# Kernel tuning notes

Hardware: AMD Instinct MI355X
Metric: run time of the kernel (lower is better)

Reference implementation:

```python
import jax, jax.numpy as jnp
import numpy as np

# Standard SMPL kinematic tree (24 joints); parents[0] = -1 (root)
PARENTS = np.array([-1, 0, 0, 0, 1, 2, 3, 4, 5, 6, 7, 8, 9, 9, 9, 12, 13, 14, 16, 17, 18, 19, 20, 21], dtype=np.int32)
B, V, J, NSHAPE, NPOSEBASIS = 512, 6890, 24, 10, 207


def setup_inputs() -> dict:
    key = jax.random.key(0)
    ks = jax.random.split(key, 9)
    poses = jax.random.normal(ks[0], (B, J * 3), dtype=jnp.float32) * 0.2
    shapes = jax.random.normal(ks[1], (B, NSHAPE), dtype=jnp.float32)
    Rh = jax.random.normal(ks[2], (B, 3), dtype=jnp.float32) * 0.2
    Th = jax.random.normal(ks[3], (B, 3), dtype=jnp.float32)
    v_template = jax.random.normal(ks[4], (V, 3), dtype=jnp.float32)
    shapedirs = jax.random.normal(ks[5], (V, 3, NSHAPE), dtype=jnp.float32) * 0.01
    posedirs = jax.random.normal(ks[6], (NPOSEBASIS, V * 3), dtype=jnp.float32) * 0.01
    jr = jax.random.uniform(ks[7], (J, V), dtype=jnp.float32)
    J_regressor = jr / jnp.sum(jr, axis=1, keepdims=True)
    w = jax.random.uniform(ks[8], (V, J), dtype=jnp.float32)
    weights = w / jnp.sum(w, axis=1, keepdims=True)
    return {"poses": poses, "shapes": shapes, "Rh": Rh, "Th": Th,
            "v_template": v_template, "shapedirs": shapedirs, "posedirs": posedirs,
            "J_regressor": J_regressor, "weights": weights}


def batch_rodrigues(rot_vecs):
    # rot_vecs: (N,3) -> (N,3,3); matches smplx batch_rodrigues
    angle = jnp.linalg.norm(rot_vecs + 1e-8, axis=1, keepdims=True)  # (N,1)
    rd = rot_vecs / angle
    cos = jnp.cos(angle)[:, :, None]
    sin = jnp.sin(angle)[:, :, None]
    rx, ry, rz = rd[:, 0], rd[:, 1], rd[:, 2]
    zeros = jnp.zeros_like(rx)
    K = jnp.stack([zeros, -rz, ry, rz, zeros, -rx, -ry, rx, zeros], axis=1).reshape(-1, 3, 3)
    ident = jnp.eye(3, dtype=rot_vecs.dtype)[None]
    return ident + sin * K + (1.0 - cos) * jnp.matmul(K, K)


def smpl_forward(poses, shapes, Rh, Th, v_template, shapedirs, posedirs, J_regressor, weights):
    bn = poses.shape[0]
    # shape blendshapes: v_shaped (B,V,3)
    v_shaped = v_template[None] + jnp.einsum('bl,vdl->bvd', shapes, shapedirs)
    # rest-pose joints (B,J,3)
    Jrest = jnp.einsum('jv,bvd->bjd', J_regressor, v_shaped)
    # per-joint rotation matrices
    rot_mats = batch_rodrigues(poses.reshape(-1, 3)).reshape(bn, J, 3, 3)
    # pose blendshapes
    ident = jnp.eye(3, dtype=poses.dtype)
    pose_feature = (rot_mats[:, 1:] - ident).reshape(bn, -1)  # (B,207)
    v_posed = v_shaped + jnp.matmul(pose_feature, posedirs).reshape(bn, V, 3)
    # kinematic chain rigid transforms
    rel_joints = jnp.concatenate([Jrest[:, :1], Jrest[:, 1:] - Jrest[:, PARENTS[1:]]], axis=1)
    bottom = jnp.tile(jnp.array([0., 0., 0., 1.], dtype=poses.dtype), (bn, J, 1, 1))
    tmats = jnp.concatenate([jnp.concatenate([rot_mats, rel_joints[..., None]], axis=-1), bottom], axis=-2)  # (B,J,4,4)
    chain = [tmats[:, 0]]
    for i in range(1, J):
        chain.append(jnp.matmul(chain[PARENTS[i]], tmats[:, i]))
    transforms = jnp.stack(chain, axis=1)  # (B,J,4,4)
    # remove rest-pose joint location from transforms
    tj = jnp.einsum('bjik,bjk->bji', transforms[:, :, :3, :3], Jrest)
    A = transforms.at[:, :, :3, 3].add(-tj)
    # linear blend skinning
    T = jnp.einsum('vj,bjik->bvik', weights, A)  # (B,V,4,4)
    verts = jnp.einsum('bvik,bvk->bvi', T[:, :, :3, :3], v_posed) + T[:, :, :3, 3]
    # global rotation + translation
    rot = batch_rodrigues(Rh)  # (B,3,3)
    vertices = jnp.einsum('bij,bvj->bvi', rot, verts) + Th[:, None]
    return vertices


def reference(poses, shapes, Rh, Th, v_template, shapedirs, posedirs, J_regressor, weights):
    return smpl_forward(poses, shapes, Rh, Th, v_template, shapedirs, posedirs, J_regressor, weights)
```

## Files before the change

### kernel.cpp

```cpp
#include <hip/hip_runtime.h>


#define BN 512
#define NV 6890
#define NVP 6912
#define NJ 24
#define NS 10
#define NP 207
#define PSTR 208
#define KP 224
#define NPAD 20736
#define BB 8
#define TV 256

#define WS_JSP 0
#define WS_G   6400
#define WS_PF  153856
#define WS_A1  12800
#define WS_A2  127488
#define WS_WT  324096
#define WS_BT  545280
#define FULL_NEED ((size_t)10380288)

typedef unsigned short u16;
typedef short bf16x8 __attribute__((ext_vector_type(8)));
typedef float f32x4  __attribute__((ext_vector_type(4)));

__constant__ int c_par[NJ] = {-1,0,0,0,1,2,3,4,5,6,7,8,9,9,9,12,13,14,16,17,18,19,20,21};

__device__ __forceinline__ u16 f2bf(float f){
    union { float f; unsigned i; } x; x.f = f;
    unsigned r = x.i + 0x7fffu + ((x.i >> 16) & 1u);
    return (u16)(r >> 16);
}

__global__ __launch_bounds__(256) void k_prep(const float* __restrict__ jreg,
                                              const float* __restrict__ vt,
                                              const float* __restrict__ sd,
                                              const float* __restrict__ pd,
                                              const float* __restrict__ wts,
                                              float* __restrict__ ws,
                                              u16* __restrict__ bt,
                                              u16* __restrict__ wt,
                                              int full){
    __shared__ __align__(16) float s_red[4][33];
    __shared__ __align__(16) u16 s_tile[32][65];
    int bid = blockIdx.x;
    int t = threadIdx.x;

    if(bid < 192){
        int j = bid >> 3, s = bid & 7;
        int v0 = s*864, v1 = min(NV, v0+864);
        float acc[33];
        #pragma unroll
        for(int k=0;k<33;k++) acc[k]=0.f;
        for(int v=v0+t; v<v1; v+=256){
            float jr = jreg[j*NV+v];
            #pragma unroll
            for(int d=0;d<3;d++) acc[d] = fmaf(jr, vt[v*3+d], acc[d]);
            const float2* sp = (const float2*)(sd + (size_t)v*30);
            #pragma unroll
            for(int k=0;k<15;k++){
                float2 s2 = sp[k];
                acc[3+2*k]   = fmaf(jr, s2.x, acc[3+2*k]);
                acc[3+2*k+1] = fmaf(jr, s2.y, acc[3+2*k+1]);
            }
        }
        int lane = t & 63, wv = t >> 6;
        #pragma unroll
        for(int k=0;k<33;k++){
            float val = acc[k];
            #pragma unroll
            for(int off=32; off; off>>=1) val += __shfl_down(val, off, 64);
            if(lane==0) s_red[wv][k]=val;
        }
        __syncthreads();
        if(t<33) ws[WS_JSP + (j*8+s)*33 + t] = s_red[0][t]+s_red[1][t]+s_red[2][t]+s_red[3][t];
    } else if(bid < 2460){
        if(!full) return;
        int bid2 = bid - 192;
        int n0 = (bid2 % 324) * 64;
        int k0 = (bid2 / 324) * 32;
        int nl = t & 63, kb = (t>>6)*8;
        int n = n0 + nl;
        #pragma unroll
        for(int i=0;i<8;i++){
            int k = k0 + kb + i;
            float v = 0.f;
            if(n < NV*3){
                if(k < NP)           v = pd[(size_t)k*(NV*3) + n];
                else if(k < NP+NS)   v = sd[(size_t)(n/3)*30 + (n%3)*10 + (k-NP)];
            }
            s_tile[kb+i][nl] = f2bf(v);
        }
        __syncthreads();
        int nl2 = t >> 2, kc = t & 3;
        union { u16 s[8]; uint4 q; } u;
        #pragma unroll
        for(int i=0;i<8;i++) u.s[i] = s_tile[kc*8+i][nl2];
        int ng = n0 + nl2;
        int v = ng/3, d = ng%3;
        int chunk = (k0>>3) + kc;
        *(uint4*)(bt + (((size_t)d*28 + chunk)*NVP + v)*8) = u.q;
    } else {
        if(!full) return;
        int v = (bid - 2460)*256 + t;
        if(v >= NVP) return;
        union { u16 s[32]; uint4 q[4]; } u;
        #pragma unroll
        for(int j=0;j<24;j++) u.s[j] = (v<NV) ? f2bf(wts[(size_t)v*24+j]) : (u16)0;
        #pragma unroll
        for(int j=24;j<32;j++) u.s[j]=0;
        #pragma unroll
        for(int c=0;c<4;c++)
            *(uint4*)(wt + ((size_t)c*NVP + v)*8) = u.q[c];
    }
}

__global__ __launch_bounds__(64) void k_chain(const float* __restrict__ poses,
                                              const float* __restrict__ shapes,
                                              const float* __restrict__ Rh,
                                              float* __restrict__ ws,
                                              u16* __restrict__ a1,
                                              u16* __restrict__ a2,
                                              int full){
    int b = blockIdx.x;
    int t = threadIdx.x;
    __shared__ float R[25][9];
    __shared__ float sh[NS];
    __shared__ float js[792];
    __shared__ float jrest[NJ][3];
    __shared__ float rel[NJ][3];
    __shared__ float chR[NJ][9];
    __shared__ float chT[NJ][3];
    __shared__ float Gs[NJ][12];

    if(t<25){
        float x,y,z;
        if(t<24){ x=poses[b*72+t*3]; y=poses[b*72+t*3+1]; z=poses[b*72+t*3+2]; }
        else    { x=Rh[b*3];         y=Rh[b*3+1];         z=Rh[b*3+2]; }
        float ax=x+1e-8f, ay=y+1e-8f, az=z+1e-8f;
        float ang = sqrtf(ax*ax+ay*ay+az*az);
        float inv = 1.f/ang;
        float rx=x*inv, ry=y*inv, rz=z*inv;
        float s = sinf(ang), c = cosf(ang), oc = 1.f - c;
        R[t][0]=1.f+oc*(-rz*rz-ry*ry); R[t][1]=-s*rz+oc*(rx*ry);      R[t][2]= s*ry+oc*(rx*rz);
        R[t][3]= s*rz+oc*(rx*ry);      R[t][4]=1.f+oc*(-rz*rz-rx*rx); R[t][5]=-s*rx+oc*(ry*rz);
        R[t][6]=-s*ry+oc*(rx*rz);      R[t][7]= s*rx+oc*(ry*rz);      R[t][8]=1.f+oc*(-ry*ry-rx*rx);
    }
    if(t<NS) sh[t]=shapes[b*NS+t];
    for(int idx=t; idx<792; idx+=64){
        int j = idx/33, e = idx%33;
        float a = 0.f;
        #pragma unroll
        for(int s=0;s<8;s++) a += ws[WS_JSP + (j*8+s)*33 + e];
        js[idx]=a;
    }
    __syncthreads();

    for(int idx=t; idx<KP; idx+=64){
        float v = 0.f;
        if(idx<NP){
            int j = 1 + idx/9, e = idx%9;
            v = R[j][e] - ((e==0||e==4||e==8)?1.f:0.f);
        } else if(idx<NP+NS) v = sh[idx-NP];
        if(full){ a1[(((size_t)(idx>>3))*BN + b)*8 + (idx&7)] = f2bf(v); }
        else if(idx<PSTR) ws[WS_PF + b*PSTR + idx] = (idx<NP)?v:0.f;
    }
    if(t<NJ){
        #pragma unroll
        for(int d=0;d<3;d++){
            float a = js[t*33 + d];
            #pragma unroll
            for(int l=0;l<NS;l++) a = fmaf(sh[l], js[t*33 + 3 + d*10 + l], a);
            jrest[t][d]=a;
        }
    }
    __syncthreads();
    if(t<NJ){
        int p = c_par[t];
        #pragma unroll
        for(int d=0;d<3;d++) rel[t][d] = (t==0) ? jrest[0][d] : jrest[t][d]-jrest[p][d];
    }
    __syncthreads();
    if(t<9) chR[0][t]=R[0][t];
    if(t<3) chT[0][t]=rel[0][t];
    __syncthreads();
    for(int i=1;i<NJ;i++){
        if(t<12){
            int r=t>>2, cc=t&3, p=c_par[i];
            if(cc<3){
                chR[i][r*3+cc] = chR[p][r*3+0]*R[i][0*3+cc] + chR[p][r*3+1]*R[i][1*3+cc] + chR[p][r*3+2]*R[i][2*3+cc];
            } else {
                chT[i][r] = chR[p][r*3+0]*rel[i][0] + chR[p][r*3+1]*rel[i][1] + chR[p][r*3+2]*rel[i][2] + chT[p][r];
            }
        }
        __syncthreads();
    }
    if(t<NJ){
        float rg[9];
        #pragma unroll
        for(int k=0;k<9;k++) rg[k]=R[24][k];
        float at[3];
        #pragma unroll
        for(int r=0;r<3;r++){
            float tj = chR[t][r*3+0]*jrest[t][0] + chR[t][r*3+1]*jrest[t][1] + chR[t][r*3+2]*jrest[t][2];
            at[r] = chT[t][r] - tj;
        }
        #pragma unroll
        for(int r=0;r<3;r++){
            #pragma unroll
            for(int cc=0;cc<3;cc++)
                Gs[t][r*4+cc] = rg[r*3+0]*chR[t][0*3+cc] + rg[r*3+1]*chR[t][1*3+cc] + rg[r*3+2]*chR[t][2*3+cc];
            Gs[t][r*4+3] = rg[r*3+0]*at[0] + rg[r*3+1]*at[1] + rg[r*3+2]*at[2];
        }
    }
    __syncthreads();
    if(full){
        for(int idx=t; idx<12*32; idx+=64){
            int e = idx>>5, k = idx&31;
            float v = (k<NJ) ? Gs[k][e] : 0.f;
            a2[((((size_t)e*4)+(k>>3))*BN + b)*8 + (k&7)] = f2bf(v);
        }
    } else if(t<NJ){
        float* g = &ws[WS_G + b*288 + t*12];
        #pragma unroll
        for(int e=0;e<12;e++) g[e] = Gs[t][e];
    }
}

__global__ __launch_bounds__(256) void k_fused(const u16* __restrict__ A1,
                                               const u16* __restrict__ A2,
                                               const u16* __restrict__ WT,
                                               const u16* __restrict__ BT,
                                               const float* __restrict__ vt,
                                               const float* __restrict__ th,
                                               float* __restrict__ out){
    int t = threadIdx.x;
    int w = t>>6, lane = t&63;
    int quad = lane>>4, l16 = lane&15;
    int v = blockIdx.y*64 + w*16 + l16;

    bf16x8 Bf[3][7];
    #pragma unroll
    for(int d=0;d<3;d++)
        #pragma unroll
        for(int s=0;s<7;s++)
            Bf[d][s] = *(const bf16x8*)(BT + (((size_t)d*28 + s*4 + quad)*NVP + v)*8);
    bf16x8 wf = *(const bf16x8*)(WT + ((size_t)quad*NVP + v)*8);
    float vt0=0.f, vt1=0.f, vt2=0.f;
    if(v<NV){ vt0=vt[v*3]; vt1=vt[v*3+1]; vt2=vt[v*3+2]; }
    f32x4 zz = {0.f,0.f,0.f,0.f};

    #pragma unroll 1
    for(int mi=0;mi<8;mi++){
        int m0 = blockIdx.x*128 + mi*16;
        int mrow = m0 + l16;
        f32x4 accP0=zz, accP1=zz, accP2=zz;
        #pragma unroll
        for(int s=0;s<7;s++){
            bf16x8 af = *(const bf16x8*)(A1 + (((size_t)s*4 + quad)*BN + mrow)*8);
            accP0 = __builtin_amdgcn_mfma_f32_16x16x32_bf16(af, Bf[0][s], accP0, 0,0,0);
            accP1 = __builtin_amdgcn_mfma_f32_16x16x32_bf16(af, Bf[1][s], accP1, 0,0,0);
            accP2 = __builtin_amdgcn_mfma_f32_16x16x32_bf16(af, Bf[2][s], accP2, 0,0,0);
        }
        f32x4 accT[12];
        #pragma unroll
        for(int e=0;e<12;e++){
            bf16x8 gf = *(const bf16x8*)(A2 + (((size_t)e*4 + quad)*BN + mrow)*8);
            accT[e] = __builtin_amdgcn_mfma_f32_16x16x32_bf16(gf, wf, zz, 0,0,0);
        }
        if(v < NV){
            #pragma unroll
            for(int r=0;r<4;r++){
                int b = m0 + quad*4 + r;
                float t0 = th[b*3+0], t1 = th[b*3+1], t2 = th[b*3+2];
                float p0 = accP0[r] + vt0;
                float p1 = accP1[r] + vt1;
                float p2 = accP2[r] + vt2;
                float o0 = fmaf(accT[0][r],p0, fmaf(accT[1][r],p1, fmaf(accT[2][r], p2, accT[3][r]))) + t0;
                float o1 = fmaf(accT[4][r],p0, fmaf(accT[5][r],p1, fmaf(accT[6][r], p2, accT[7][r]))) + t1;
                float o2 = fmaf(accT[8][r],p0, fmaf(accT[9][r],p1, fmaf(accT[10][r],p2, accT[11][r]))) + t2;
                float* op = out + ((size_t)b*NV + v)*3;
                op[0]=o0; op[1]=o1; op[2]=o2;
            }
        }
    }
}

__global__ __launch_bounds__(256) void k_main(const float* __restrict__ vt,
                                              const float* __restrict__ sd,
                                              const float* __restrict__ pd,
                                              const float* __restrict__ wts,
                                              const float* __restrict__ th,
                                              const float* __restrict__ shapes,
                                              const float* __restrict__ ws,
                                              float* __restrict__ out){
    __shared__ __align__(16) float pf_s[BB*PSTR];
    __shared__ __align__(16) float g_s[BB*288];
    __shared__ float th_s[BB*3];
    __shared__ float sh_s[BB*NS];
    int tid = threadIdx.x;
    int b0  = blockIdx.y * BB;
    int v   = blockIdx.x * TV + tid;

    for(int i=tid; i<BB*PSTR; i+=TV) pf_s[i] = ws[WS_PF + b0*PSTR + i];
    for(int i=tid; i<BB*288;  i+=TV) g_s[i]  = ws[WS_G  + b0*288  + i];
    if(tid<BB*3)  th_s[tid] = th[b0*3+tid];
    if(tid<BB*NS) sh_s[tid] = shapes[b0*NS+tid];
    __syncthreads();
    if(v>=NV) return;

    float sdv[30];
    {
        const float2* sp = (const float2*)(sd + (size_t)v*30);
        #pragma unroll
        for(int i=0;i<15;i++){ float2 s2 = sp[i]; sdv[2*i]=s2.x; sdv[2*i+1]=s2.y; }
    }
    float vt0=vt[v*3], vt1=vt[v*3+1], vt2=vt[v*3+2];
    float vp[BB][3];
    #pragma unroll
    for(int b=0;b<BB;b++){
        #pragma unroll
        for(int d=0;d<3;d++){
            float a = (d==0)?vt0:((d==1)?vt1:vt2);
            #pragma unroll
            for(int l=0;l<NS;l++) a = fmaf(sh_s[b*NS+l], sdv[d*10+l], a);
            vp[b][d]=a;
        }
    }
    const float* pcol = pd + (size_t)v*3;
    int p=0;
    for(; p<=NP-4; p+=4){
        float pdv[4][3];
        #pragma unroll
        for(int q=0;q<4;q++){
            size_t base = (size_t)(p+q)*(NV*3);
            pdv[q][0]=pcol[base]; pdv[q][1]=pcol[base+1]; pdv[q][2]=pcol[base+2];
        }
        #pragma unroll
        for(int b=0;b<BB;b++){
            float4 f = *(const float4*)&pf_s[b*PSTR+p];
            #pragma unroll
            for(int d=0;d<3;d++)
                vp[b][d] = fmaf(f.x,pdv[0][d], fmaf(f.y,pdv[1][d], fmaf(f.z,pdv[2][d], fmaf(f.w,pdv[3][d], vp[b][d]))));
        }
    }
    for(; p<NP; p++){
        size_t base=(size_t)p*(NV*3);
        float p0=pcol[base], p1=pcol[base+1], p2=pcol[base+2];
        #pragma unroll
        for(int b=0;b<BB;b++){
            float f = pf_s[b*PSTR+p];
            vp[b][0]=fmaf(f,p0,vp[b][0]); vp[b][1]=fmaf(f,p1,vp[b][1]); vp[b][2]=fmaf(f,p2,vp[b][2]);
        }
    }
    float w[24];
    {
        const float4* wp = (const float4*)(wts + (size_t)v*24);
        #pragma unroll
        for(int i=0;i<6;i++){
            float4 u = wp[i];
            w[i*4+0]=u.x; w[i*4+1]=u.y; w[i*4+2]=u.z; w[i*4+3]=u.w;
        }
    }
    #pragma unroll 1
    for(int b=0;b<BB;b++){
        float4 T0=make_float4(0.f,0.f,0.f,0.f), T1=T0, T2=T0;
        #pragma unroll
        for(int j=0;j<NJ;j++){
            float wj = w[j];
            const float4* g = (const float4*)&g_s[b*288 + j*12];
            float4 g0=g[0], g1=g[1], g2=g[2];
            T0.x=fmaf(wj,g0.x,T0.x); T0.y=fmaf(wj,g0.y,T0.y); T0.z=fmaf(wj,g0.z,T0.z); T0.w=fmaf(wj,g0.w,T0.w);
            T1.x=fmaf(wj,g1.x,T1.x); T1.y=fmaf(wj,g1.y,T1.y); T1.z=fmaf(wj,g1.z,T1.z); T1.w=fmaf(wj,g1.w,T1.w);
            T2.x=fmaf(wj,g2.x,T2.x); T2.y=fmaf(wj,g2.y,T2.y); T2.z=fmaf(wj,g2.z,T2.z); T2.w=fmaf(wj,g2.w,T2.w);
        }
        float x=vp[b][0], y=vp[b][1], z=vp[b][2];
        float ox = fmaf(T0.x,x, fmaf(T0.y,y, fmaf(T0.z,z, T0.w))) + th_s[b*3+0];
        float oy = fmaf(T1.x,x, fmaf(T1.y,y, fmaf(T1.z,z, T1.w))) + th_s[b*3+1];
        float oz = fmaf(T2.x,x, fmaf(T2.y,y, fmaf(T2.z,z, T2.w))) + th_s[b*3+2];
        size_t o = ((size_t)(b0+b)*NV + v)*3;
        out[o]=ox; out[o+1]=oy; out[o+2]=oz;
    }
}

extern "C" void kernel_launch(void* const* d_in, const int* in_sizes, int n_in,
                              void* d_out, int out_size, void* d_ws, size_t ws_size,
                              hipStream_t stream){
    const float* poses  = (const float*)d_in[0];
    const float* shapes = (const float*)d_in[1];
    const float* Rh     = (const float*)d_in[2];
    const float* Th     = (const float*)d_in[3];
    const float* vt     = (const float*)d_in[4];
    const float* sd     = (const float*)d_in[5];
    const float* pdirs  = (const float*)d_in[6];
    const float* jreg   = (const float*)d_in[7];
    const float* wts    = (const float*)d_in[8];
    float* ws  = (float*)d_ws;
    float* out = (float*)d_out;
    u16* u = (u16*)d_ws;
    int full = (ws_size >= FULL_NEED) ? 1 : 0;

    hipLaunchKernelGGL(k_prep, dim3(2487), dim3(256), 0, stream,
                       jreg, vt, sd, pdirs, wts, ws, u + WS_BT, u + WS_WT, full);
    hipLaunchKernelGGL(k_chain, dim3(BN), dim3(64), 0, stream, poses, shapes, Rh, ws,
                       u + WS_A1, u + WS_A2, full);
    if(full){
        hipLaunchKernelGGL(k_fused, dim3(BN/128, NVP/64), dim3(256), 0, stream,
                           u + WS_A1, u + WS_A2, u + WS_WT, u + WS_BT, vt, Th, out);
    } else {
        hipLaunchKernelGGL(k_main, dim3((NV+TV-1)/TV, BN/BB), dim3(256), 0, stream,
                           vt, sd, pdirs, wts, Th, shapes, ws, out);
    }
}
```

Before: 137.4 us.

## Parallelize kinematic chain by tree level and pack four batches per block

The chain kernel now computes all joints at the same tree depth together, so it runs 8 level steps instead of 23 serial joint steps with a barrier after each. It also processes four batch items per 256-thread block (one wavefront each), which amortizes the joint-regressor partial-sum reduction over four items. Separately, the prep kernel stages shapedirs rows through shared memory with coalesced float4 loads instead of strided per-thread float2 reads. The staging adds extra block barriers and a large shared buffer that may lower occupancy of the prep kernel.

```diff
diff --git a/kernel.cpp b/kernel.cpp
--- a/kernel.cpp
+++ b/kernel.cpp
@@ -27,6 +27,8 @@
 typedef float f32x4  __attribute__((ext_vector_type(4)));
 
 __constant__ int c_par[NJ] = {-1,0,0,0,1,2,3,4,5,6,7,8,9,9,9,12,13,14,16,17,18,19,20,21};
+__constant__ int c_lvl_joint[23] = {1,2,3, 4,5,6, 7,8,9, 10,11,12,13,14, 15,16,17, 18,19, 20,21, 22,23};
+__constant__ int c_lvl_off[9]    = {0,3,6,9,14,17,19,21,23};
 
 __device__ __forceinline__ u16 f2bf(float f){
     union { float f; unsigned i; } x; x.f = f;
@@ -45,6 +47,7 @@
                                               int full){
     __shared__ __align__(16) float s_red[4][33];
     __shared__ __align__(16) u16 s_tile[32][65];
+    __shared__ __align__(16) float s_sd[256*30];
     int bid = blockIdx.x;
     int t = threadIdx.x;
 
@@ -54,17 +57,22 @@
         float acc[33];
         #pragma unroll
         for(int k=0;k<33;k++) acc[k]=0.f;
-        for(int v=v0+t; v<v1; v+=256){
-            float jr = jreg[j*NV+v];
-            #pragma unroll
-            for(int d=0;d<3;d++) acc[d] = fmaf(jr, vt[v*3+d], acc[d]);
-            const float2* sp = (const float2*)(sd + (size_t)v*30);
-            #pragma unroll
-            for(int k=0;k<15;k++){
-                float2 s2 = sp[k];
-                acc[3+2*k]   = fmaf(jr, s2.x, acc[3+2*k]);
-                acc[3+2*k+1] = fmaf(jr, s2.y, acc[3+2*k+1]);
+        for(int c0=v0; c0<v1; c0+=256){
+            int nv = min(256, v1-c0);
+            int nf4 = (nv*30) >> 2;
+            const float4* src = (const float4*)(sd + (size_t)c0*30);
+            for(int i=t; i<nf4; i+=256) ((float4*)s_sd)[i] = src[i];
+            __syncthreads();
+            if(t<nv){
+                int v = c0 + t;
+                float jr = jreg[j*NV+v];
+                #pragma unroll
+                for(int d=0;d<3;d++) acc[d] = fmaf(jr, vt[v*3+d], acc[d]);
+                const float* sp = &s_sd[t*30];
+                #pragma unroll
+                for(int k=0;k<30;k++) acc[3+k] = fmaf(jr, sp[k], acc[3+k]);
             }
+            __syncthreads();
         }
         int lane = t & 63, wv = t >> 6;
         #pragma unroll
@@ -117,115 +125,131 @@
     }
 }
 
-__global__ __launch_bounds__(64) void k_chain(const float* __restrict__ poses,
-                                              const float* __restrict__ shapes,
-                                              const float* __restrict__ Rh,
-                                              float* __restrict__ ws,
-                                              u16* __restrict__ a1,
-                                              u16* __restrict__ a2,
-                                              int full){
-    int b = blockIdx.x;
-    int t = threadIdx.x;
-    __shared__ float R[25][9];
-    __shared__ float sh[NS];
+__global__ __launch_bounds__(256) void k_chain(const float* __restrict__ poses,
+                                               const float* __restrict__ shapes,
+                                               const float* __restrict__ Rh,
+                                               float* __restrict__ ws,
+                                               u16* __restrict__ a1,
+                                               u16* __restrict__ a2,
+                                               int full){
+    int tid  = threadIdx.x;
+    int w    = tid >> 6;
+    int lane = tid & 63;
+    int b    = blockIdx.x*4 + w;
+
     __shared__ float js[792];
-    __shared__ float jrest[NJ][3];
-    __shared__ float rel[NJ][3];
-    __shared__ float chR[NJ][9];
-    __shared__ float chT[NJ][3];
-    __shared__ float Gs[NJ][12];
-
-    if(t<25){
+    __shared__ float R[4][25][9];
+    __shared__ float sh[4][NS];
+    __shared__ float jrest[4][NJ][3];
+    __shared__ float rel[4][NJ][3];
+    __shared__ float chR[4][NJ][9];
+    __shared__ float chT[4][NJ][3];
+    __shared__ float Gs[4][NJ][12];
+
+    for(int idx=tid; idx<792; idx+=256){
+        int j = idx/33, e = idx%33;
+        float a = 0.f;
+        #pragma unroll
+        for(int s=0;s<8;s++) a += ws[WS_JSP + (j*8+s)*33 + e];
+        js[idx]=a;
+    }
+    if(lane<25){
         float x,y,z;
-        if(t<24){ x=poses[b*72+t*3]; y=poses[b*72+t*3+1]; z=poses[b*72+t*3+2]; }
-        else    { x=Rh[b*3];         y=Rh[b*3+1];         z=Rh[b*3+2]; }
+        if(lane<24){ x=poses[b*72+lane*3]; y=poses[b*72+lane*3+1]; z=poses[b*72+lane*3+2]; }
+        else       { x=Rh[b*3];            y=Rh[b*3+1];            z=Rh[b*3+2]; }
         float ax=x+1e-8f, ay=y+1e-8f, az=z+1e-8f;
         float ang = sqrtf(ax*ax+ay*ay+az*az);
         float inv = 1.f/ang;
         float rx=x*inv, ry=y*inv, rz=z*inv;
         float s = sinf(ang), c = cosf(ang), oc = 1.f - c;
-        R[t][0]=1.f+oc*(-rz*rz-ry*ry); R[t][1]=-s*rz+oc*(rx*ry);      R[t][2]= s*ry+oc*(rx*rz);
-        R[t][3]= s*rz+oc*(rx*ry);      R[t][4]=1.f+oc*(-rz*rz-rx*rx); R[t][5]=-s*rx+oc*(ry*rz);
-        R[t][6]=-s*ry+oc*(rx*rz);      R[t][7]= s*rx+oc*(ry*rz);      R[t][8]=1.f+oc*(-ry*ry-rx*rx);
-    }
-    if(t<NS) sh[t]=shapes[b*NS+t];
-    for(int idx=t; idx<792; idx+=64){
-        int j = idx/33, e = idx%33;
-        float a = 0.f;
-        #pragma unroll
-        for(int s=0;s<8;s++) a += ws[WS_JSP + (j*8+s)*33 + e];
-        js[idx]=a;
-    }
-    __syncthreads();
-
-    for(int idx=t; idx<KP; idx+=64){
+        R[w][lane][0]=1.f+oc*(-rz*rz-ry*ry); R[w][lane][1]=-s*rz+oc*(rx*ry);      R[w][lane][2]= s*ry+oc*(rx*rz);
+        R[w][lane][3]= s*rz+oc*(rx*ry);      R[w][lane][4]=1.f+oc*(-rz*rz-rx*rx); R[w][lane][5]=-s*rx+oc*(ry*rz);
+        R[w][lane][6]=-s*ry+oc*(rx*rz);      R[w][lane][7]= s*rx+oc*(ry*rz);      R[w][lane][8]=1.f+oc*(-ry*ry-rx*rx);
+    }
+    if(lane<NS) sh[w][lane]=shapes[b*NS+lane];
+    __syncthreads();
+
+    for(int idx=lane; idx<KP; idx+=64){
         float v = 0.f;
         if(idx<NP){
             int j = 1 + idx/9, e = idx%9;
-            v = R[j][e] - ((e==0||e==4||e==8)?1.f:0.f);
-        } else if(idx<NP+NS) v = sh[idx-NP];
+            v = R[w][j][e] - ((e==0||e==4||e==8)?1.f:0.f);
+        } else if(idx<NP+NS) v = sh[w][idx-NP];
         if(full){ a1[(((size_t)(idx>>3))*BN + b)*8 + (idx&7)] = f2bf(v); }
         else if(idx<PSTR) ws[WS_PF + b*PSTR + idx] = (idx<NP)?v:0.f;
     }
-    if(t<NJ){
+    if(lane<NJ){
         #pragma unroll
         for(int d=0;d<3;d++){
-            float a = js[t*33 + d];
-            #pragma unroll
-            for(int l=0;l<NS;l++) a = fmaf(sh[l], js[t*33 + 3 + d*10 + l], a);
-            jrest[t][d]=a;
-        }
-    }
-    __syncthreads();
-    if(t<NJ){
-        int p = c_par[t];
-        #pragma unroll
-        for(int d=0;d<3;d++) rel[t][d] = (t==0) ? jrest[0][d] : jrest[t][d]-jrest[p][d];
-    }
-    __syncthreads();
-    if(t<9) chR[0][t]=R[0][t];
-    if(t<3) chT[0][t]=rel[0][t];
-    __syncthreads();
-    for(int i=1;i<NJ;i++){
-        if(t<12){
-            int r=t>>2, cc=t&3, p=c_par[i];
+            float a = js[lane*33 + d];
+            #pragma unroll
+            for(int l=0;l<NS;l++) a = fmaf(sh[w][l], js[lane*33 + 3 + d*10 + l], a);
+            jrest[w][lane][d]=a;
+        }
+    }
+    __syncthreads();
+    if(lane<NJ){
+        int p = c_par[lane];
+        #pragma unroll
+        for(int d=0;d<3;d++) rel[w][lane][d] = (lane==0) ? jrest[w][0][d] : jrest[w][lane][d]-jrest[w][p][d];
+    }
+    __syncthreads();
+    if(lane<9) chR[w][0][lane]=R[w][0][lane];
+    if(lane<3) chT[w][0][lane]=rel[w][0][lane];
+    __syncthreads();
+    #pragma unroll
+    for(int L=0; L<8; L++){
+        int o = c_lvl_off[L];
+        int n = c_lvl_off[L+1]-o;
+        if(lane < n*12){
+            int ji = c_lvl_joint[o + lane/12];
+            int t12 = lane - (lane/12)*12;
+            int r = t12>>2, cc = t12&3, p = c_par[ji];
             if(cc<3){
-                chR[i][r*3+cc] = chR[p][r*3+0]*R[i][0*3+cc] + chR[p][r*3+1]*R[i][1*3+cc] + chR[p][r*3+2]*R[i][2*3+cc];
+                chR[w][ji][r*3+cc] = chR[w][p][r*3+0]*R[w][ji][0*3+cc]
+                                   + chR[w][p][r*3+1]*R[w][ji][1*3+cc]
+                                   + chR[w][p][r*3+2]*R[w][ji][2*3+cc];
             } else {
-                chT[i][r] = chR[p][r*3+0]*rel[i][0] + chR[p][r*3+1]*rel[i][1] + chR[p][r*3+2]*rel[i][2] + chT[p][r];
+                chT[w][ji][r] = chR[w][p][r*3+0]*rel[w][ji][0]
+                              + chR[w][p][r*3+1]*rel[w][ji][1]
+                              + chR[w][p][r*3+2]*rel[w][ji][2] + chT[w][p][r];
             }
         }
         __syncthreads();
     }
-    if(t<NJ){
+    if(lane<NJ){
         float rg[9];
         #pragma unroll
-        for(int k=0;k<9;k++) rg[k]=R[24][k];
+        for(int k=0;k<9;k++) rg[k]=R[w][24][k];
         float at[3];
         #pragma unroll
         for(int r=0;r<3;r++){
-            float tj = chR[t][r*3+0]*jrest[t][0] + chR[t][r*3+1]*jrest[t][1] + chR[t][r*3+2]*jrest[t][2];
-            at[r] = chT[t][r] - tj;
+            float tj = chR[w][lane][r*3+0]*jrest[w][lane][0]
+                     + chR[w][lane][r*3+1]*jrest[w][lane][1]
+                     + chR[w][lane][r*3+2]*jrest[w][lane][2];
+            at[r] = chT[w][lane][r] - tj;
         }
         #pragma unroll
         for(int r=0;r<3;r++){
             #pragma unroll
             for(int cc=0;cc<3;cc++)
-                Gs[t][r*4+cc] = rg[r*3+0]*chR[t][0*3+cc] + rg[r*3+1]*chR[t][1*3+cc] + rg[r*3+2]*chR[t][2*3+cc];
-            Gs[t][r*4+3] = rg[r*3+0]*at[0] + rg[r*3+1]*at[1] + rg[r*3+2]*at[2];
+                Gs[w][lane][r*4+cc] = rg[r*3+0]*chR[w][lane][0*3+cc]
+                                    + rg[r*3+1]*chR[w][lane][1*3+cc]
+                                    + rg[r*3+2]*chR[w][lane][2*3+cc];
+            Gs[w][lane][r*4+3] = rg[r*3+0]*at[0] + rg[r*3+1]*at[1] + rg[r*3+2]*at[2];
         }
     }
     __syncthreads();
     if(full){
-        for(int idx=t; idx<12*32; idx+=64){
+        for(int idx=lane; idx<12*32; idx+=64){
             int e = idx>>5, k = idx&31;
-            float v = (k<NJ) ? Gs[k][e] : 0.f;
+            float v = (k<NJ) ? Gs[w][k][e] : 0.f;
             a2[((((size_t)e*4)+(k>>3))*BN + b)*8 + (k&7)] = f2bf(v);
         }
-    } else if(t<NJ){
-        float* g = &ws[WS_G + b*288 + t*12];
-        #pragma unroll
-        for(int e=0;e<12;e++) g[e] = Gs[t][e];
+    } else if(lane<NJ){
+        float* g = &ws[WS_G + b*288 + lane*12];
+        #pragma unroll
+        for(int e=0;e<12;e++) g[e] = Gs[w][lane][e];
     }
 }
 
@@ -404,7 +428,7 @@
 
     hipLaunchKernelGGL(k_prep, dim3(2487), dim3(256), 0, stream,
                        jreg, vt, sd, pdirs, wts, ws, u + WS_BT, u + WS_WT, full);
-    hipLaunchKernelGGL(k_chain, dim3(BN), dim3(64), 0, stream, poses, shapes, Rh, ws,
+    hipLaunchKernelGGL(k_chain, dim3(BN/4), dim3(256), 0, stream, poses, shapes, Rh, ws,
                        u + WS_A1, u + WS_A2, full);
     if(full){
         hipLaunchKernelGGL(k_fused, dim3(BN/128, NVP/64), dim3(256), 0, stream,
```

Result: no change. 139.6 us (+1.6%).
